# Kernel optimization log

Measured on AMD Instinct MI355X. Metric: run time of the kernel, lower is better.

Reference implementation:

```python
import jax, jax.numpy as jnp
import numpy as np

DIM = 256
NEG_SLOPE = 0.01  # torch F.leaky_relu default


def setup_inputs() -> dict:
    key = jax.random.key(0)
    ks = jax.random.split(key, 10)
    B, O, I, D = 16, 64, 512, DIM
    q = jax.random.normal(ks[0], (B, O, D), dtype=jnp.float32)
    k = jax.random.normal(ks[1], (B, I, D), dtype=jnp.float32)
    v = jax.random.normal(ks[2], (B, I, D), dtype=jnp.float32)
    mask = jax.random.randint(ks[3], (B, I), 0, 2).astype(bool)  # 1/True = pad
    s = 1.0 / np.sqrt(2 * D)
    # score MLP: Linear(2D -> D), tanh, Linear(D -> 1)
    W1 = jax.random.normal(ks[4], (D, 2 * D), dtype=jnp.float32) * s
    b1 = jnp.zeros((D,), dtype=jnp.float32)
    W2 = jax.random.normal(ks[5], (1, D), dtype=jnp.float32) * (1.0 / np.sqrt(D))
    b2 = jnp.zeros((1,), dtype=jnp.float32)
    # output projection fw: Linear(D -> D)
    Wf = jax.random.normal(ks[6], (D, D), dtype=jnp.float32) * (1.0 / np.sqrt(D))
    bf = jnp.zeros((D,), dtype=jnp.float32)
    return {"q": q, "k": k, "v": v, "mask": mask,
            "W1": W1, "b1": b1, "W2": W2, "b2": b2, "Wf": Wf, "bf": bf}


def reference(q, k, v, mask, W1, b1, W2, b2, Wf, bf):
    # Linear over concat([q, k]) decomposes exactly: W1 @ [q;k] = W1q@q + W1k@k
    D = q.shape[-1]
    W1q, W1k = W1[:, :D], W1[:, D:]
    qp = jnp.einsum('bod,hd->boh', q, W1q)          # (B, O, D)
    kp = jnp.einsum('bid,hd->bih', k, W1k)          # (B, I, D)
    h = jnp.tanh(qp[:, :, None, :] + kp[:, None, :, :] + b1)  # (B, O, I, D)
    score = jnp.einsum('boih,h->boi', h, W2[0]) + b2[0]       # (B, O, I)
    score = jnp.where(mask[:, None, :], -jnp.inf, score)
    attn = jax.nn.softmax(score, axis=-1)           # (B, O, I)
    out = jnp.einsum('boi,bid->bod', attn, v)       # (B, O, D)
    out = out @ Wf.T + bf                           # dropout in eval mode = identity
    out = jnp.where(out >= 0, out, NEG_SLOPE * out) # leaky_relu
    return out, attn
```

## Files before the change

kernel.cpp:

```cpp
#include <hip/hip_runtime.h>
#include <math.h>

#define DIM 256
#define BATCH 16
#define NO 64
#define NI 512
#define NEG_SLOPE 0.01f
#define CSCALE 2.885390081777927f
#define OT 4

typedef float f32x4 __attribute__((ext_vector_type(4)));
typedef __bf16 bf16x8 __attribute__((ext_vector_type(8)));
typedef unsigned int u32x4 __attribute__((ext_vector_type(4)));

__device__ __forceinline__ void split2(float f, unsigned int& hi16, float& lo) {
  unsigned int u = __builtin_bit_cast(unsigned int, f);
  unsigned int h = (u + 0x7FFFu + ((u >> 16) & 1u)) & 0xFFFF0000u;
  hi16 = h >> 16;
  lo = f - __builtin_bit_cast(float, h);
}
__device__ __forceinline__ unsigned int rne16(float f) {
  unsigned int u = __builtin_bit_cast(unsigned int, f);
  return (u + 0x7FFFu + ((u >> 16) & 1u)) >> 16;
}

struct __align__(8) U2 { unsigned int x, y; };

#define OFF_AH 0
#define OFF_AL 9216
#define OFF_WH 18432
#define OFF_WL 27648

__global__ __launch_bounds__(256, 4) void proj_kernel(
    const float* __restrict__ q, const float* __restrict__ k,
    const float* __restrict__ W1, const float* __restrict__ b1,
    const float* __restrict__ Wf, const int* __restrict__ mask,
    float* __restrict__ Eq, float* __restrict__ Ek4, float* __restrict__ WfT)
{
  __shared__ __align__(16) char smemRaw[36864];
  __shared__ int idx_s[64];
  __shared__ int swtot[4];

  const int t  = threadIdx.x;
  const int bx = blockIdx.x;

  if (bx >= 576) {
    float* smem = (float*)smemRaw;
    const int tt = bx - 576;
    const int tr = tt >> 2, tc = tt & 3;
#pragma unroll
    for (int p = 0; p < 4; ++p) {
      int idx2 = p * 256 + t;
      int row = idx2 >> 4, j = idx2 & 15;
      float4 vv = *(const float4*)(Wf + (size_t)(tr * 64 + row) * 256 + tc * 64 + j * 4);
      *(float4*)&smem[row * 68 + j * 4] = vv;
    }
    __syncthreads();
#pragma unroll
    for (int p = 0; p < 4; ++p) {
      int idx2 = p * 256 + t;
      int row = idx2 >> 4, j = idx2 & 15;
      float4 ov;
      ov.x = smem[(j * 4 + 0) * 68 + row];
      ov.y = smem[(j * 4 + 1) * 68 + row];
      ov.z = smem[(j * 4 + 2) * 68 + row];
      ov.w = smem[(j * 4 + 3) * 68 + row];
      *(float4*)(WfT + (size_t)(tc * 64 + row) * 256 + tr * 64 + j * 4) = ov;
    }
    return;
  }

  const int mt = bx >> 2;
  const int nt = bx & 3;
  const int h0 = nt * 64;
  const bool isq = (mt < 16);

  const int srow = t >> 4;
  const int sc4  = t & 15;
  const int lane = t & 63, w = t >> 6;
  const int m0w = (w >> 1) * 32, n0w = (w & 1) * 32;
  const int lr = lane & 15, lg = lane >> 4;

  const float* src;
  int coff, bb = 0, jb0 = 0, cntb = 0;
  int rowg[4];

  if (isq) {
    src  = q + (size_t)(mt * 64) * DIM;
    coff = 0;
#pragma unroll
    for (int p = 0; p < 4; ++p) rowg[p] = srow + p * 16;
  } else {
    const int ki = mt - 16;
    bb  = ki >> 3;
    jb0 = (ki & 7) * 64;
    const int e0 = (mask[bb * NI + 2 * t] == 0);
    const int e1 = (mask[bb * NI + 2 * t + 1] == 0);
    const int ps = e0 + e1;
    int x = ps;
#pragma unroll
    for (int off = 1; off < 64; off <<= 1) {
      int y = __shfl_up(x, off, 64);
      if (lane >= off) x += y;
    }
    if (lane == 63) swtot[w] = x;
    if (t < 64) idx_s[t] = 0;
    __syncthreads();
    int woffv = 0;
#pragma unroll
    for (int w2 = 0; w2 < 4; ++w2) {
      int v_ = swtot[w2];
      if (w2 < w) woffv += v_;
      cntb += v_;
    }
    const int excl = woffv + x - ps;
    const int p0 = excl, p1 = excl + e0;
    if (e0 && p0 >= jb0 && p0 < jb0 + 64) idx_s[p0 - jb0] = 2 * t;
    if (e1 && p1 >= jb0 && p1 < jb0 + 64) idx_s[p1 - jb0] = 2 * t + 1;
    __syncthreads();
    if (jb0 >= cntb) return;
    src  = k + (size_t)bb * NI * DIM;
    coff = DIM;
#pragma unroll
    for (int p = 0; p < 4; ++p) rowg[p] = idx_s[srow + p * 16];
  }

  f32x4 acc[2][2] = {};

  float4 aR[4], wR[4];
#define LOADC(c0_)                                                              \
  _Pragma("unroll")                                                             \
  for (int p = 0; p < 4; ++p) {                                                 \
    aR[p] = *(const float4*)(src + (size_t)rowg[p] * DIM + (c0_) + sc4 * 4);    \
    wR[p] = *(const float4*)(W1 + (size_t)(h0 + srow + p * 16) * (2 * DIM) + coff + (c0_) + sc4 * 4); \
  }

  LOADC(0)

  for (int c = 0; c < 4; ++c) {
#pragma unroll
    for (int p = 0; p < 4; ++p) {
      int row = srow + p * 16;
      int boff = row * 144 + sc4 * 8;
      unsigned int h0_, h1_, h2_, h3_;
      float l0, l1, l2, l3;
      split2(aR[p].x, h0_, l0); split2(aR[p].y, h1_, l1);
      split2(aR[p].z, h2_, l2); split2(aR[p].w, h3_, l3);
      *(U2*)(smemRaw + OFF_AH + boff) = { h0_ | (h1_ << 16), h2_ | (h3_ << 16) };
      *(U2*)(smemRaw + OFF_AL + boff) = { rne16(l0) | (rne16(l1) << 16),
                                          rne16(l2) | (rne16(l3) << 16) };
      split2(wR[p].x, h0_, l0); split2(wR[p].y, h1_, l1);
      split2(wR[p].z, h2_, l2); split2(wR[p].w, h3_, l3);
      *(U2*)(smemRaw + OFF_WH + boff) = { h0_ | (h1_ << 16), h2_ | (h3_ << 16) };
      *(U2*)(smemRaw + OFF_WL + boff) = { rne16(l0) | (rne16(l1) << 16),
                                          rne16(l2) | (rne16(l3) << 16) };
    }
    __syncthreads();

    if (c < 3) { LOADC((c + 1) * 64) }

#pragma unroll
    for (int kk = 0; kk < 2; ++kk) {
      const int kb = kk * 64 + lg * 16;
      bf16x8 ah[2], al[2], bh[2], bl[2];
#pragma unroll
      for (int mi = 0; mi < 2; ++mi) {
        int row = m0w + mi * 16 + lr;
        ah[mi] = __builtin_bit_cast(bf16x8, *(const u32x4*)(smemRaw + OFF_AH + row * 144 + kb));
        al[mi] = __builtin_bit_cast(bf16x8, *(const u32x4*)(smemRaw + OFF_AL + row * 144 + kb));
      }
#pragma unroll
      for (int ni = 0; ni < 2; ++ni) {
        int row = n0w + ni * 16 + lr;
        bh[ni] = __builtin_bit_cast(bf16x8, *(const u32x4*)(smemRaw + OFF_WH + row * 144 + kb));
        bl[ni] = __builtin_bit_cast(bf16x8, *(const u32x4*)(smemRaw + OFF_WL + row * 144 + kb));
      }
#pragma unroll
      for (int mi = 0; mi < 2; ++mi)
#pragma unroll
        for (int ni = 0; ni < 2; ++ni) {
          acc[mi][ni] = __builtin_amdgcn_mfma_f32_16x16x32_bf16(ah[mi], bh[ni], acc[mi][ni], 0, 0, 0);
          acc[mi][ni] = __builtin_amdgcn_mfma_f32_16x16x32_bf16(ah[mi], bl[ni], acc[mi][ni], 0, 0, 0);
          acc[mi][ni] = __builtin_amdgcn_mfma_f32_16x16x32_bf16(al[mi], bh[ni], acc[mi][ni], 0, 0, 0);
        }
    }
    __syncthreads();
  }

  if (isq) {
    const int r0 = mt * 64;
#pragma unroll
    for (int ni = 0; ni < 2; ++ni) {
      int h = h0 + n0w + ni * 16 + lr;
      float b1v = b1[h];
#pragma unroll
      for (int mi = 0; mi < 2; ++mi)
#pragma unroll
        for (int rg = 0; rg < 4; ++rg) {
          int r = r0 + m0w + mi * 16 + lg * 4 + rg;
          Eq[(size_t)r * DIM + h] =
              __builtin_amdgcn_exp2f((acc[mi][ni][rg] + b1v) * CSCALE);
        }
    }
  } else {
    const int lim = cntb - jb0;
#pragma unroll
    for (int mi = 0; mi < 2; ++mi)
#pragma unroll
      for (int rg = 0; rg < 4; ++rg) {
        int local = m0w + mi * 16 + lg * 4 + rg;
        if (local < lim) {
          int pos = jb0 + local;
#pragma unroll
          for (int ni = 0; ni < 2; ++ni) {
            int h = h0 + n0w + ni * 16 + lr;
            Ek4[((size_t)(bb * 64 + (h >> 2)) * NI + pos) * 4 + (h & 3)] =
                __builtin_amdgcn_exp2f(acc[mi][ni][rg] * CSCALE);
          }
        }
      }
  }
}

__device__ __forceinline__ void f4arr(float4 v, float* a) {
  a[0] = v.x; a[1] = v.y; a[2] = v.z; a[3] = v.w;
}

__global__ __launch_bounds__(512, 2) void attn_kernel(
    const float* __restrict__ Eq, const float* __restrict__ Ek4,
    const float* __restrict__ v, const int* __restrict__ mask,
    const float* __restrict__ W2, const float* __restrict__ b2,
    const float* __restrict__ WfT, const float* __restrict__ bf,
    float* __restrict__ out, float* __restrict__ attn_out)
{
  __shared__ float sc[OT][NI];
  __shared__ int   idxs[NI];
  __shared__ float qs[OT][DIM];
  __shared__ float pvp[8][OT][DIM];
  __shared__ float o0[OT][DIM];
  __shared__ float red4[8][OT];
  __shared__ float redw[8];
  __shared__ int   swtot8[8];

  const int t    = threadIdx.x;
  const int lane = t & 63;
  const int wid  = t >> 6;

  const int blk  = blockIdx.x;
  const int tile = (blk & 7) * 32 + (blk >> 3);
  const int b    = tile >> 4;
  const int bo0  = b * 64 + (tile & 15) * OT;

  const int unm = (mask[b * NI + t] == 0) ? 1 : 0;
  unsigned long long bal = __ballot(unm);
  int my = __popcll(bal & ((1ull << lane) - 1ull));
  if (lane == 0) swtot8[wid] = __popcll(bal);

  if (t < 256) {
    const int r = t >> 6, part = t & 63;
    *(float4*)&qs[r][part * 4] =
        *(const float4*)(Eq + (size_t)(bo0 + r) * DIM + part * 4);
  }

  float partial = (t < DIM) ? W2[t] : 0.f;
#pragma unroll
  for (int off = 32; off >= 1; off >>= 1) partial += __shfl_xor(partial, off, 64);
  if (lane == 0) redw[wid] = partial;
  __syncthreads();

  int cntb = 0, woffv = 0;
#pragma unroll
  for (int w = 0; w < 8; ++w) {
    int v_ = swtot8[w];
    if (w < wid) woffv += v_;
    cntb += v_;
  }
  const int myPos = unm ? (woffv + my) : -1;
  if (unm) idxs[myPos] = t;

  float sumw2 = 0.f;
#pragma unroll
  for (int w = 0; w < 8; ++w) sumw2 += redw[w];
  const float base = sumw2 + b2[0];

  const int j = t;
  const bool active = (j < cntb);
  const int jc = active ? j : (cntb > 0 ? cntb - 1 : 0);
  const float4* kb4 = (const float4*)Ek4 + (size_t)b * 64 * NI;

  float accv[OT] = {};
  if (wid * 64 < cntb) {
#pragma unroll 4
    for (int hq = 0; hq < 64; ++hq) {
      float4 kq = kb4[(size_t)hq * NI + jc];
      float wr[4], kv[4];
      f4arr(*(const float4*)(W2 + hq * 4), wr);
      f4arr(kq, kv);
      float qr[OT][4];
#pragma unroll
      for (int r = 0; r < OT; ++r) f4arr(*(const float4*)&qs[r][hq * 4], qr[r]);
#pragma unroll
      for (int pr = 0; pr < 2; ++pr) {
        const int ea = pr * 2, eb = pr * 2 + 1;
#pragma unroll
        for (int r = 0; r < OT; ++r) {
          float A = fmaf(qr[r][ea], kv[ea], 1.f);
          float B = fmaf(qr[r][eb], kv[eb], 1.f);
          float N = fmaf(wr[eb], A, wr[ea] * B);
          accv[r] = fmaf(N, __builtin_amdgcn_rcpf(A * B), accv[r]);
        }
      }
    }
  }

  float p[OT], psum[OT];
#pragma unroll
  for (int r = 0; r < OT; ++r) {
    float s = active ? (base - 2.f * accv[r]) : -INFINITY;
    p[r] = __builtin_amdgcn_exp2f(s * 1.4426950408889634f);
    psum[r] = p[r];
  }
#pragma unroll
  for (int off = 32; off >= 1; off >>= 1)
#pragma unroll
    for (int r = 0; r < OT; ++r) psum[r] += __shfl_xor(psum[r], off, 64);
  __syncthreads();
  if (lane == 0)
#pragma unroll
    for (int r = 0; r < OT; ++r) red4[wid][r] = psum[r];
  __syncthreads();
  float ss[OT] = {};
#pragma unroll
  for (int w = 0; w < 8; ++w)
#pragma unroll
    for (int r = 0; r < OT; ++r) ss[r] += red4[w][r];
#pragma unroll
  for (int r = 0; r < OT; ++r)
    sc[r][j] = p[r] * __builtin_amdgcn_rcpf(ss[r]);
  __syncthreads();

#pragma unroll
  for (int r = 0; r < OT; ++r) {
    float wv = (myPos >= 0) ? sc[r][myPos] : 0.f;
    attn_out[(size_t)(bo0 + r) * NI + t] = wv;
  }

  {
    const int d4 = lane;
    float4 av[OT] = {};
    const float4* vb4 = (const float4*)(v + (size_t)b * NI * DIM);
    const int jend = min(wid * 64 + 64, cntb);
#pragma unroll 2
    for (int jb = wid * 64; jb < jend; ++jb) {
      int row = idxs[jb];
      float sa[OT];
#pragma unroll
      for (int r = 0; r < OT; ++r) sa[r] = sc[r][jb];
      float4 vv = vb4[(size_t)row * 64 + d4];
#pragma unroll
      for (int r = 0; r < OT; ++r) {
        av[r].x = fmaf(sa[r], vv.x, av[r].x);
        av[r].y = fmaf(sa[r], vv.y, av[r].y);
        av[r].z = fmaf(sa[r], vv.z, av[r].z);
        av[r].w = fmaf(sa[r], vv.w, av[r].w);
      }
    }
#pragma unroll
    for (int r = 0; r < OT; ++r)
      *(float4*)&pvp[wid][r][d4 * 4] = av[r];
  }
  __syncthreads();
  {
    const int ob = t >> 8, d = t & 255;
#pragma unroll
    for (int g = 0; g < 2; ++g) {
      int oo = ob + g * 2;
      float sacc = 0.f;
#pragma unroll
      for (int w = 0; w < 8; ++w) sacc += pvp[w][oo][d];
      o0[oo][d] = sacc;
    }
  }
  __syncthreads();

  if (t < DIM) {
    const int d = t;
    float f[OT] = {};
#pragma unroll 8
    for (int e4 = 0; e4 < 64; ++e4) {
      float oa[OT][4];
#pragma unroll
      for (int r = 0; r < OT; ++r) f4arr(*(const float4*)&o0[r][e4 * 4], oa[r]);
#pragma unroll
      for (int c = 0; c < 4; ++c) {
        float wv = WfT[(size_t)(e4 * 4 + c) * DIM + d];
#pragma unroll
        for (int r = 0; r < OT; ++r) f[r] = fmaf(oa[r][c], wv, f[r]);
      }
    }
    float bfv = bf[d];
#pragma unroll
    for (int r = 0; r < OT; ++r) {
      float fv = f[r] + bfv;
      fv = (fv >= 0.f) ? fv : NEG_SLOPE * fv;
      out[(size_t)(bo0 + r) * DIM + d] = fv;
    }
  }
}

extern "C" void kernel_launch(void* const* d_in, const int* in_sizes, int n_in,
                              void* d_out, int out_size, void* d_ws, size_t ws_size,
                              hipStream_t stream) {
  const float* q    = (const float*)d_in[0];
  const float* k    = (const float*)d_in[1];
  const float* v    = (const float*)d_in[2];
  const int*   mask = (const int*)d_in[3];
  const float* W1   = (const float*)d_in[4];
  const float* b1   = (const float*)d_in[5];
  const float* W2   = (const float*)d_in[6];
  const float* b2   = (const float*)d_in[7];
  const float* Wf   = (const float*)d_in[8];
  const float* bf   = (const float*)d_in[9];

  float* out      = (float*)d_out;
  float* attn_out = out + (size_t)BATCH * NO * DIM;

  float* Eq   = (float*)d_ws;
  float* Ek4  = Eq + (size_t)BATCH * NO * DIM;
  float* WfT  = Ek4 + (size_t)BATCH * DIM * NI;

  proj_kernel<<<592, 256, 0, stream>>>(q, k, W1, b1, Wf, mask, Eq, Ek4, WfT);
  attn_kernel<<<(BATCH * NO) / OT, 512, 0, stream>>>(Eq, Ek4, v, mask,
                                                     W2, b2, WfT, bf, out, attn_out);
}
```

Measured before the change: 131.1 us.

## Double attn block size, split score reduction across lane quads, parallelize output projection

Raises the attention kernel to 1024 threads per block. Each key column's score is computed by four lanes, each summing a quarter of the hidden dimension, and the partials are combined with shuffles. The PV accumulation now spreads over 16 waves, and the final Wf projection uses all threads with float4 weight loads and a shuffle reduction. W2 is cached in LDS. This gives more parallelism per CU, since there is only one block per CU, at the cost of less coalesced key loads, more shared memory and extra shuffles.

```diff
diff --git a/kernel.cpp b/kernel.cpp
--- a/kernel.cpp
+++ b/kernel.cpp
@@ -226,7 +226,7 @@
   a[0] = v.x; a[1] = v.y; a[2] = v.z; a[3] = v.w;
 }
 
-__global__ __launch_bounds__(512, 2) void attn_kernel(
+__global__ __launch_bounds__(1024, 4) void attn_kernel(
     const float* __restrict__ Eq, const float* __restrict__ Ek4,
     const float* __restrict__ v, const int* __restrict__ mask,
     const float* __restrict__ W2, const float* __restrict__ b2,
@@ -235,11 +235,13 @@
 {
   __shared__ float sc[OT][NI];
   __shared__ int   idxs[NI];
+  __shared__ int   posa[NI];
   __shared__ float qs[OT][DIM];
-  __shared__ float pvp[8][OT][DIM];
+  __shared__ float w2s[DIM];
+  __shared__ float pvp[16][OT][DIM];
   __shared__ float o0[OT][DIM];
-  __shared__ float red4[8][OT];
-  __shared__ float redw[8];
+  __shared__ float red8[16][OT];
+  __shared__ float redw[16];
   __shared__ int   swtot8[8];
 
   const int t    = threadIdx.x;
@@ -251,15 +253,18 @@
   const int b    = tile >> 4;
   const int bo0  = b * 64 + (tile & 15) * OT;
 
-  const int unm = (mask[b * NI + t] == 0) ? 1 : 0;
+  const int unm = (t < NI) ? ((mask[b * NI + t] == 0) ? 1 : 0) : 0;
   unsigned long long bal = __ballot(unm);
   int my = __popcll(bal & ((1ull << lane) - 1ull));
-  if (lane == 0) swtot8[wid] = __popcll(bal);
+  if (lane == 0 && wid < 8) swtot8[wid] = __popcll(bal);
 
   if (t < 256) {
     const int r = t >> 6, part = t & 63;
     *(float4*)&qs[r][part * 4] =
         *(const float4*)(Eq + (size_t)(bo0 + r) * DIM + part * 4);
+  } else if (t < 320) {
+    const int part = t - 256;
+    *(float4*)&w2s[part * 4] = *(const float4*)(W2 + part * 4);
   }
 
   float partial = (t < DIM) ? W2[t] : 0.f;
@@ -277,133 +282,168 @@
   }
   const int myPos = unm ? (woffv + my) : -1;
   if (unm) idxs[myPos] = t;
+  if (t < NI) posa[t] = myPos;
 
   float sumw2 = 0.f;
 #pragma unroll
-  for (int w = 0; w < 8; ++w) sumw2 += redw[w];
+  for (int w = 0; w < 16; ++w) sumw2 += redw[w];
   const float base = sumw2 + b2[0];
 
-  const int j = t;
-  const bool active = (j < cntb);
-  const int jc = active ? j : (cntb > 0 ? cntb - 1 : 0);
   const float4* kb4 = (const float4*)Ek4 + (size_t)b * 64 * NI;
-
-  float accv[OT] = {};
-  if (wid * 64 < cntb) {
+  const int quad = lane >> 2;
+  const int hqb  = (lane & 3) << 4;
+  float psum[OT] = {};
+  float pval[2][OT];
+  int   pcol[2] = {-1, -1};
+
+#pragma unroll
+  for (int pass = 0; pass < 2; ++pass) {
+    const int pb = pass << 8;
+    if (pb + (wid << 4) < cntb) {
+      const int jc0 = pb + (wid << 4) + quad;
+      const bool act = jc0 < cntb;
+      const int jc = act ? jc0 : (cntb - 1);
+      float a[OT] = {};
 #pragma unroll 4
-    for (int hq = 0; hq < 64; ++hq) {
-      float4 kq = kb4[(size_t)hq * NI + jc];
-      float wr[4], kv[4];
-      f4arr(*(const float4*)(W2 + hq * 4), wr);
-      f4arr(kq, kv);
-      float qr[OT][4];
-#pragma unroll
-      for (int r = 0; r < OT; ++r) f4arr(*(const float4*)&qs[r][hq * 4], qr[r]);
-#pragma unroll
-      for (int pr = 0; pr < 2; ++pr) {
-        const int ea = pr * 2, eb = pr * 2 + 1;
-#pragma unroll
-        for (int r = 0; r < OT; ++r) {
-          float A = fmaf(qr[r][ea], kv[ea], 1.f);
-          float B = fmaf(qr[r][eb], kv[eb], 1.f);
-          float N = fmaf(wr[eb], A, wr[ea] * B);
-          accv[r] = fmaf(N, __builtin_amdgcn_rcpf(A * B), accv[r]);
+      for (int hh = 0; hh < 16; ++hh) {
+        const int hq = hqb + hh;
+        float4 kq = kb4[(size_t)hq * NI + jc];
+        float wr[4], kv[4];
+        f4arr(*(const float4*)&w2s[hq * 4], wr);
+        f4arr(kq, kv);
+        float qr[OT][4];
+#pragma unroll
+        for (int r = 0; r < OT; ++r) f4arr(*(const float4*)&qs[r][hq * 4], qr[r]);
+#pragma unroll
+        for (int pr = 0; pr < 2; ++pr) {
+          const int ea = pr * 2, eb = pr * 2 + 1;
+#pragma unroll
+          for (int r = 0; r < OT; ++r) {
+            float A = fmaf(qr[r][ea], kv[ea], 1.f);
+            float B = fmaf(qr[r][eb], kv[eb], 1.f);
+            float N = fmaf(wr[eb], A, wr[ea] * B);
+            a[r] = fmaf(N, __builtin_amdgcn_rcpf(A * B), a[r]);
+          }
         }
       }
-    }
-  }
-
-  float p[OT], psum[OT];
+#pragma unroll
+      for (int r = 0; r < OT; ++r) {
+        a[r] += __shfl_xor(a[r], 1, 64);
+        a[r] += __shfl_xor(a[r], 2, 64);
+        float s = act ? (base - 2.f * a[r]) : -INFINITY;
+        float p = __builtin_amdgcn_exp2f(s * 1.4426950408889634f);
+        psum[r] += p;
+        pval[pass][r] = p;
+        sc[r][jc0] = p;
+      }
+      pcol[pass] = jc0;
+    }
+  }
+
+#pragma unroll
+  for (int off = 32; off >= 1; off >>= 1)
+#pragma unroll
+    for (int r = 0; r < OT; ++r) psum[r] += __shfl_xor(psum[r], off, 64);
+  if (lane == 0)
+#pragma unroll
+    for (int r = 0; r < OT; ++r) red8[wid][r] = psum[r];
+  __syncthreads();
+  float inv[OT];
 #pragma unroll
   for (int r = 0; r < OT; ++r) {
-    float s = active ? (base - 2.f * accv[r]) : -INFINITY;
-    p[r] = __builtin_amdgcn_exp2f(s * 1.4426950408889634f);
-    psum[r] = p[r];
-  }
-#pragma unroll
-  for (int off = 32; off >= 1; off >>= 1)
-#pragma unroll
-    for (int r = 0; r < OT; ++r) psum[r] += __shfl_xor(psum[r], off, 64);
+    float ssr = 0.f;
+#pragma unroll
+    for (int w = 0; w < 16; ++w) ssr += red8[w][r];
+    inv[r] = __builtin_amdgcn_rcpf(0.25f * ssr);
+  }
+#pragma unroll
+  for (int pass = 0; pass < 2; ++pass) {
+    if (pcol[pass] >= 0) {
+#pragma unroll
+      for (int r = 0; r < OT; ++r) sc[r][pcol[pass]] = pval[pass][r] * inv[r];
+    }
+  }
   __syncthreads();
-  if (lane == 0)
-#pragma unroll
-    for (int r = 0; r < OT; ++r) red4[wid][r] = psum[r];
-  __syncthreads();
-  float ss[OT] = {};
-#pragma unroll
-  for (int w = 0; w < 8; ++w)
-#pragma unroll
-    for (int r = 0; r < OT; ++r) ss[r] += red4[w][r];
-#pragma unroll
-  for (int r = 0; r < OT; ++r)
-    sc[r][j] = p[r] * __builtin_amdgcn_rcpf(ss[r]);
-  __syncthreads();
-
-#pragma unroll
-  for (int r = 0; r < OT; ++r) {
-    float wv = (myPos >= 0) ? sc[r][myPos] : 0.f;
-    attn_out[(size_t)(bo0 + r) * NI + t] = wv;
-  }
 
   {
-    const int d4 = lane;
+    const int i = t & (NI - 1);
+    const int rb = (t >> 9) << 1;
+    const int pi = posa[i];
+#pragma unroll
+    for (int rr = 0; rr < 2; ++rr) {
+      float wv = (pi >= 0) ? sc[rb + rr][pi] : 0.f;
+      attn_out[(size_t)(bo0 + rb + rr) * NI + i] = wv;
+    }
+  }
+
+  {
     float4 av[OT] = {};
     const float4* vb4 = (const float4*)(v + (size_t)b * NI * DIM);
-    const int jend = min(wid * 64 + 64, cntb);
-#pragma unroll 2
-    for (int jb = wid * 64; jb < jend; ++jb) {
-      int row = idxs[jb];
-      float sa[OT];
-#pragma unroll
-      for (int r = 0; r < OT; ++r) sa[r] = sc[r][jb];
-      float4 vv = vb4[(size_t)row * 64 + d4];
-#pragma unroll
-      for (int r = 0; r < OT; ++r) {
-        av[r].x = fmaf(sa[r], vv.x, av[r].x);
-        av[r].y = fmaf(sa[r], vv.y, av[r].y);
-        av[r].z = fmaf(sa[r], vv.z, av[r].z);
-        av[r].w = fmaf(sa[r], vv.w, av[r].w);
+#pragma unroll
+    for (int pass = 0; pass < 2; ++pass) {
+      const int start = (pass << 8) + (wid << 4);
+      const int jend = min(start + 16, cntb);
+#pragma unroll 4
+      for (int jb = start; jb < jend; ++jb) {
+        int row = idxs[jb];
+        float sa[OT];
+#pragma unroll
+        for (int r = 0; r < OT; ++r) sa[r] = sc[r][jb];
+        float4 vv = vb4[(size_t)row * 64 + lane];
+#pragma unroll
+        for (int r = 0; r < OT; ++r) {
+          av[r].x = fmaf(sa[r], vv.x, av[r].x);
+          av[r].y = fmaf(sa[r], vv.y, av[r].y);
+          av[r].z = fmaf(sa[r], vv.z, av[r].z);
+          av[r].w = fmaf(sa[r], vv.w, av[r].w);
+        }
       }
     }
 #pragma unroll
     for (int r = 0; r < OT; ++r)
-      *(float4*)&pvp[wid][r][d4 * 4] = av[r];
+      *(float4*)&pvp[wid][r][lane * 4] = av[r];
   }
   __syncthreads();
   {
-    const int ob = t >> 8, d = t & 255;
-#pragma unroll
-    for (int g = 0; g < 2; ++g) {
-      int oo = ob + g * 2;
-      float sacc = 0.f;
-#pragma unroll
-      for (int w = 0; w < 8; ++w) sacc += pvp[w][oo][d];
-      o0[oo][d] = sacc;
-    }
+    const int oo = t >> 8, d = t & 255;
+    float sacc = 0.f;
+#pragma unroll
+    for (int w = 0; w < 16; ++w) sacc += pvp[w][oo][d];
+    o0[oo][d] = sacc;
   }
   __syncthreads();
 
-  if (t < DIM) {
-    const int d = t;
-    float f[OT] = {};
+  {
+    const int oo   = wid >> 2;
+    const int dblk = (wid & 3) * 64;
+    const int dq   = lane & 15;
+    const int eg   = lane >> 4;
+    const int d0   = dblk + dq * 4;
+    const int e0   = eg * 64;
+    float f[4] = {};
 #pragma unroll 8
-    for (int e4 = 0; e4 < 64; ++e4) {
-      float oa[OT][4];
-#pragma unroll
-      for (int r = 0; r < OT; ++r) f4arr(*(const float4*)&o0[r][e4 * 4], oa[r]);
-#pragma unroll
-      for (int c = 0; c < 4; ++c) {
-        float wv = WfT[(size_t)(e4 * 4 + c) * DIM + d];
-#pragma unroll
-        for (int r = 0; r < OT; ++r) f[r] = fmaf(oa[r][c], wv, f[r]);
-      }
-    }
-    float bfv = bf[d];
-#pragma unroll
-    for (int r = 0; r < OT; ++r) {
-      float fv = f[r] + bfv;
-      fv = (fv >= 0.f) ? fv : NEG_SLOPE * fv;
-      out[(size_t)(bo0 + r) * DIM + d] = fv;
+    for (int ee = 0; ee < 64; ++ee) {
+      const int e = e0 + ee;
+      float wv[4];
+      f4arr(*(const float4*)&WfT[(size_t)e * DIM + d0], wv);
+      float ov = o0[oo][e];
+#pragma unroll
+      for (int c = 0; c < 4; ++c) f[c] = fmaf(ov, wv[c], f[c]);
+    }
+#pragma unroll
+    for (int c = 0; c < 4; ++c) {
+      f[c] += __shfl_xor(f[c], 16, 64);
+      f[c] += __shfl_xor(f[c], 32, 64);
+    }
+    if (lane < 16) {
+      float bv[4];
+      f4arr(*(const float4*)(bf + d0), bv);
+      float4 ov4;
+      float r0 = f[0] + bv[0]; ov4.x = (r0 >= 0.f) ? r0 : NEG_SLOPE * r0;
+      float r1 = f[1] + bv[1]; ov4.y = (r1 >= 0.f) ? r1 : NEG_SLOPE * r1;
+      float r2 = f[2] + bv[2]; ov4.z = (r2 >= 0.f) ? r2 : NEG_SLOPE * r2;
+      float r3 = f[3] + bv[3]; ov4.w = (r3 >= 0.f) ? r3 : NEG_SLOPE * r3;
+      *(float4*)(out + (size_t)(bo0 + oo) * DIM + d0) = ov4;
     }
   }
 }
@@ -430,6 +470,6 @@
   float* WfT  = Ek4 + (size_t)BATCH * DIM * NI;
 
   proj_kernel<<<592, 256, 0, stream>>>(q, k, W1, b1, Wf, mask, Eq, Ek4, WfT);
-  attn_kernel<<<(BATCH * NO) / OT, 512, 0, stream>>>(Eq, Ek4, v, mask,
-                                                     W2, b2, WfT, bf, out, attn_out);
-}
+  attn_kernel<<<(BATCH * NO) / OT, 1024, 0, stream>>>(Eq, Ek4, v, mask,
+                                                      W2, b2, WfT, bf, out, attn_out);
+}
```

After: 123.4 us. -5.9%, faster.
